# Performance work log

Measured on AMD Instinct MI355X. Metric: run time of the kernel, lower is better.

Reference implementation:

```python
import jax, jax.numpy as jnp
import numpy as np
import math

# Production-scale dims
B, C, H, W = 16, 3, 224, 224
STEPS = 32
T0, T1 = 0.0, 1.0
BETA = 0.1
IMPULSE = 1.0 / (abs(BETA) * math.sqrt(math.pi))
TSEQ = jnp.linspace(T0, T1, STEPS)  # sublevel thresholds


def _build_cells(x):
    """V-construction cubical complex over each [H,W] map.
    Cells: pixels (dim0, sign +1), horizontal/vertical edges (dim1, sign -1),
    unit squares (dim2, sign +1). Filtration value of a cell = max over its
    incident pixels (sublevel set / lower-star filtration).
    Returns (vals [B,C,N], pix [B,C,N] argmax pixel id, sign [N]).
    """
    b, c, h, w = x.shape
    hw = h * w
    pid = jnp.arange(hw, dtype=jnp.int32).reshape(h, w)
    # vertices (+1)
    v_vals = x.reshape(b, c, hw)
    v_pix = jnp.broadcast_to(pid.reshape(hw), (b, c, hw))
    # horizontal edges (-1)
    l, r = x[..., :, :-1], x[..., :, 1:]
    h_vals = jnp.maximum(l, r).reshape(b, c, -1)
    h_pix = jnp.where(l >= r, pid[:, :-1], pid[:, 1:]).reshape(b, c, -1)
    # vertical edges (-1)
    u, d = x[..., :-1, :], x[..., 1:, :]
    ve_vals = jnp.maximum(u, d).reshape(b, c, -1)
    ve_pix = jnp.where(u >= d, pid[:-1, :], pid[1:, :]).reshape(b, c, -1)
    # squares (+1): max over 2x2 block, track argmax corner pixel
    sq = jnp.stack([x[..., :-1, :-1], x[..., :-1, 1:], x[..., 1:, :-1], x[..., 1:, 1:]], axis=-1)
    sq_vals = sq.max(-1)
    am = sq.argmax(-1)
    pids = jnp.stack([pid[:-1, :-1], pid[:-1, 1:], pid[1:, :-1], pid[1:, 1:]], axis=-1)  # [h-1,w-1,4]
    sq_pix = jnp.take_along_axis(jnp.broadcast_to(pids, sq.shape), am[..., None], axis=-1)[..., 0]
    sq_vals = sq_vals.reshape(b, c, -1)
    sq_pix = sq_pix.reshape(b, c, -1)
    vals = jnp.concatenate([v_vals, h_vals, ve_vals, sq_vals], axis=-1)
    pix = jnp.concatenate([v_pix, h_pix, ve_pix, sq_pix], axis=-1).astype(jnp.int32)
    sign = jnp.concatenate([
        jnp.ones(v_vals.shape[-1], x.dtype),
        -jnp.ones(h_vals.shape[-1], x.dtype),
        -jnp.ones(ve_vals.shape[-1], x.dtype),
        jnp.ones(sq_vals.shape[-1], x.dtype),
    ])
    return vals, pix, sign


def _ecc_forward(x):
    """ECC(t_k) = sum over cells of sign * 1[filtration_value <= t_k],
    computed via value-bucketing + scatter-add + cumulative sum.
    Returns (ecc [B, C*STEPS], residuals for backward)."""
    b, c = x.shape[0], x.shape[1]
    vals, pix, sign = _build_cells(x)
    # first threshold index k with TSEQ[k] >= f; cells with f > T1 never appear
    bins = jnp.searchsorted(TSEQ, vals, side='left')  # [B,C,N]
    mask = bins < STEPS
    bins_c = jnp.minimum(bins, STEPS - 1)
    contrib = jnp.where(mask, sign, jnp.zeros((), x.dtype))  # [B,C,N]
    n = vals.shape[-1]
    rows = jnp.arange(b * c, dtype=jnp.int32)[:, None]
    hist = jnp.zeros((b * c, STEPS), x.dtype).at[rows, bins_c.reshape(b * c, n)].add(
        contrib.reshape(b * c, n))
    ecc = jnp.cumsum(hist, axis=-1)  # Euler characteristic curve
    return ecc.reshape(b, c * STEPS), (pix, bins, mask, sign)


def setup_inputs() -> dict:
    key = jax.random.key(0)
    x = jax.random.uniform(key, (B, C, H, W), dtype=jnp.float32)
    return {"x": x}


def reference(x):
    # sublevel=True -> no negation; postprocess = Identity; output flattened [B, C*STEPS]
    ecc, _ = _ecc_forward(x)
    return ecc
```

## Files before the change

### kernel.cpp

```cpp
#include <hip/hip_runtime.h>

#define H_ 224
#define W_ 224
#define NIMG 48
#define NBINS 33
#define JOBS_PER_IMG 112
#define NBLK (NIMG * JOBS_PER_IMG / 4)
#define BLKS_PER_IMG (JOBS_PER_IMG / 4)

__device__ __forceinline__ int bin_of(float x) {
    const float C = 1.0f / 31.0f;
    int k = (int)__builtin_ceilf(x * 31.0f);
    k = min(k, 32);
    if ((float)(k - 1) * C >= x) --k;
    else if ((float)k * C < x) ++k;
    return k;
}

__global__ __launch_bounds__(256) void ecc_hist(const float* __restrict__ x,
                                                int* __restrict__ gh) {
    __shared__ int hist[4][NBINS];
    const int tid = threadIdx.x;
    const int wave = tid >> 6;
    const int lane = tid & 63;

    if (lane < NBINS) hist[wave][lane] = 0;

    const int job  = blockIdx.x * 4 + wave;
    const int img  = job / JOBS_PER_IMG;
    const int jj   = job % JOBS_PER_IMG;
    const int rowg = jj >> 2;
    const int colg = jj & 3;
    const int col  = colg * 63 + lane;
    const bool produce = (lane < 63) && (col < W_);
    const bool hasR    = produce && (col < W_ - 1);
    const int  colc    = min(col, W_ - 1);

    const float* base = x + (size_t)img * (H_ * W_) + (size_t)(rowg * 8) * W_ + colc;
    int* hw = hist[wave];

    int bcur = bin_of(base[0]);
    const int r0 = rowg * 8;

#pragma unroll
    for (int ri = 0; ri < 8; ++ri) {
        const bool hasD = (r0 + ri < H_ - 1);
        int bnext = hasD ? bin_of(base[(ri + 1) * W_]) : 0;
        int sh = __shfl_down(bcur | (bnext << 16), 1, 64);
        int bR = sh & 0xffff, bDR = sh >> 16;
        if (hasD) {
            int e1 = max(bcur, bR);
            int e2 = max(bcur, bnext);
            if (hasR) {
                int lo = min(e1, e2), hi = max(e1, e2);
                int sq = max(hi, bDR);
                if (bcur != lo) { atomicAdd(&hw[bcur], 1); atomicAdd(&hw[lo], -1); }
                if (sq != hi)   { atomicAdd(&hw[sq], 1);   atomicAdd(&hw[hi], -1); }
            } else if (produce) {
                if (bcur != e2) { atomicAdd(&hw[bcur], 1); atomicAdd(&hw[e2], -1); }
            }
        } else {
            int e1 = max(bcur, bR);
            if (hasR) {
                if (bcur != e1) { atomicAdd(&hw[bcur], 1); atomicAdd(&hw[e1], -1); }
            } else if (produce) {
                atomicAdd(&hw[bcur], 1);
            }
        }
        bcur = bnext;
    }
    __syncthreads();

    if (tid < NBINS) {
        gh[blockIdx.x * NBINS + tid] =
            hist[0][tid] + hist[1][tid] + hist[2][tid] + hist[3][tid];
    }
}

__global__ __launch_bounds__(64) void ecc_final(const int* __restrict__ gh,
                                                float* __restrict__ out) {
    const int img = blockIdx.x;
    const int lane = threadIdx.x;
    if (lane < 32) {
        int v = 0;
        const int* base = gh + img * BLKS_PER_IMG * NBINS + lane;
#pragma unroll
        for (int s = 0; s < BLKS_PER_IMG; ++s) v += base[s * NBINS];
        for (int off = 1; off < 32; off <<= 1) {
            int n = __shfl_up(v, off, 64);
            if (lane >= off) v += n;
        }
        out[img * 32 + lane] = (float)v;
    }
}

extern "C" void kernel_launch(void* const* d_in, const int* in_sizes, int n_in,
                              void* d_out, int out_size, void* d_ws, size_t ws_size,
                              hipStream_t stream) {
    const float* x = (const float*)d_in[0];
    float* out = (float*)d_out;
    int* gh = (int*)d_ws;

    ecc_hist<<<NBLK, 256, 0, stream>>>(x, gh);
    ecc_final<<<NIMG, 64, 0, stream>>>(gh, out);
}
```

Baseline: 12.56 us.

## Fuse histogram and scan into one block-per-image kernel

Replaces the two-kernel scheme (many small histogram blocks writing partials to workspace, then a per-image reduce/scan kernel) with one 1024-thread block per image. Each of the 16 waves covers 56 rows of a column strip, and the block reduces the wave histograms in shared memory before doing the prefix scan. This removes the second launch and the global workspace round trip. In exchange, only 48 blocks run, so few compute units are used and each wave walks a much longer serial row loop.

```diff
diff --git a/kernel.cpp b/kernel.cpp
--- a/kernel.cpp
+++ b/kernel.cpp
@@ -4,9 +4,8 @@
 #define W_ 224
 #define NIMG 48
 #define NBINS 33
-#define JOBS_PER_IMG 112
-#define NBLK (NIMG * JOBS_PER_IMG / 4)
-#define BLKS_PER_IMG (JOBS_PER_IMG / 4)
+#define NW 16
+#define ROWS_PER 56
 
 __device__ __forceinline__ int bin_of(float x) {
     const float C = 1.0f / 31.0f;
@@ -17,33 +16,31 @@
     return k;
 }
 
-__global__ __launch_bounds__(256) void ecc_hist(const float* __restrict__ x,
-                                                int* __restrict__ gh) {
-    __shared__ int hist[4][NBINS];
+__global__ __launch_bounds__(1024) void ecc_fused(const float* __restrict__ x,
+                                                  float* __restrict__ out) {
+    __shared__ int hist[NW][NBINS];
     const int tid = threadIdx.x;
     const int wave = tid >> 6;
     const int lane = tid & 63;
 
     if (lane < NBINS) hist[wave][lane] = 0;
 
-    const int job  = blockIdx.x * 4 + wave;
-    const int img  = job / JOBS_PER_IMG;
-    const int jj   = job % JOBS_PER_IMG;
-    const int rowg = jj >> 2;
-    const int colg = jj & 3;
+    const int img  = blockIdx.x;
+    const int rowg = wave >> 2;
+    const int colg = wave & 3;
     const int col  = colg * 63 + lane;
     const bool produce = (lane < 63) && (col < W_);
     const bool hasR    = produce && (col < W_ - 1);
     const int  colc    = min(col, W_ - 1);
+    const int  r0      = rowg * ROWS_PER;
 
-    const float* base = x + (size_t)img * (H_ * W_) + (size_t)(rowg * 8) * W_ + colc;
+    const float* base = x + (size_t)img * (H_ * W_) + (size_t)r0 * W_ + colc;
     int* hw = hist[wave];
 
     int bcur = bin_of(base[0]);
-    const int r0 = rowg * 8;
 
-#pragma unroll
-    for (int ri = 0; ri < 8; ++ri) {
+#pragma unroll 8
+    for (int ri = 0; ri < ROWS_PER; ++ri) {
         const bool hasD = (r0 + ri < H_ - 1);
         int bnext = hasD ? bin_of(base[(ri + 1) * W_]) : 0;
         int sh = __shfl_down(bcur | (bnext << 16), 1, 64);
@@ -71,26 +68,15 @@
     }
     __syncthreads();
 
-    if (tid < NBINS) {
-        gh[blockIdx.x * NBINS + tid] =
-            hist[0][tid] + hist[1][tid] + hist[2][tid] + hist[3][tid];
-    }
-}
-
-__global__ __launch_bounds__(64) void ecc_final(const int* __restrict__ gh,
-                                                float* __restrict__ out) {
-    const int img = blockIdx.x;
-    const int lane = threadIdx.x;
-    if (lane < 32) {
+    if (tid < 32) {
         int v = 0;
-        const int* base = gh + img * BLKS_PER_IMG * NBINS + lane;
 #pragma unroll
-        for (int s = 0; s < BLKS_PER_IMG; ++s) v += base[s * NBINS];
+        for (int w = 0; w < NW; ++w) v += hist[w][tid];
         for (int off = 1; off < 32; off <<= 1) {
             int n = __shfl_up(v, off, 64);
-            if (lane >= off) v += n;
+            if (tid >= off) v += n;
         }
-        out[img * 32 + lane] = (float)v;
+        out[img * 32 + tid] = (float)v;
     }
 }
 
@@ -99,8 +85,5 @@
                               hipStream_t stream) {
     const float* x = (const float*)d_in[0];
     float* out = (float*)d_out;
-    int* gh = (int*)d_ws;
-
-    ecc_hist<<<NBLK, 256, 0, stream>>>(x, gh);
-    ecc_final<<<NIMG, 64, 0, stream>>>(gh, out);
+    ecc_fused<<<NIMG, 1024, 0, stream>>>(x, out);
 }
```

Result: slower. 25.71 us (+104.6%).

## Fuse histogram and final scan into one kernel with flag-based sync

Applied to the files above, without the earlier changes.

Merges the per-block histogram kernel and the per-image reduce/scan kernel into a single launch. Each block publishes its partial histogram and then sets a release flag. The first 48 blocks spin on the flags of their image's blocks before doing the reduction and prefix scan. This removes the second launch and the gap between kernels, but relies on co-residency of all blocks. The flags are also never reset between calls, so on repeat calls stale flags can let a reader proceed before the current partials are written.

```diff
diff --git a/kernel.cpp b/kernel.cpp
--- a/kernel.cpp
+++ b/kernel.cpp
@@ -5,8 +5,10 @@
 #define NIMG 48
 #define NBINS 33
 #define JOBS_PER_IMG 112
-#define NBLK (NIMG * JOBS_PER_IMG / 4)
-#define BLKS_PER_IMG (JOBS_PER_IMG / 4)
+#define WPB 4
+#define NBLK (NIMG * JOBS_PER_IMG / WPB)
+#define BLKS_PER_IMG (JOBS_PER_IMG / WPB)
+#define MAGIC 0x5ECCD0DE
 
 __device__ __forceinline__ int bin_of(float x) {
     const float C = 1.0f / 31.0f;
@@ -17,16 +19,19 @@
     return k;
 }
 
-__global__ __launch_bounds__(256) void ecc_hist(const float* __restrict__ x,
-                                                int* __restrict__ gh) {
-    __shared__ int hist[4][NBINS];
+__global__ __launch_bounds__(256) void ecc_onepass(const float* __restrict__ x,
+                                                   int* __restrict__ gh,
+                                                   int* __restrict__ flags,
+                                                   float* __restrict__ out) {
+    __shared__ int hist[WPB][NBINS];
     const int tid = threadIdx.x;
     const int wave = tid >> 6;
     const int lane = tid & 63;
 
     if (lane < NBINS) hist[wave][lane] = 0;
 
-    const int job  = blockIdx.x * 4 + wave;
+    const int blk  = blockIdx.x;
+    const int job  = blk * WPB + wave;
     const int img  = job / JOBS_PER_IMG;
     const int jj   = job % JOBS_PER_IMG;
     const int rowg = jj >> 2;
@@ -72,25 +77,36 @@
     __syncthreads();
 
     if (tid < NBINS) {
-        gh[blockIdx.x * NBINS + tid] =
+        gh[blk * NBINS + tid] =
             hist[0][tid] + hist[1][tid] + hist[2][tid] + hist[3][tid];
     }
-}
+    __syncthreads();
 
-__global__ __launch_bounds__(64) void ecc_final(const int* __restrict__ gh,
-                                                float* __restrict__ out) {
-    const int img = blockIdx.x;
-    const int lane = threadIdx.x;
-    if (lane < 32) {
-        int v = 0;
-        const int* base = gh + img * BLKS_PER_IMG * NBINS + lane;
+    if (tid == 0) {
+        __threadfence();
+        __hip_atomic_store(&flags[blk], MAGIC, __ATOMIC_RELEASE,
+                           __HIP_MEMORY_SCOPE_AGENT);
+    }
+
+    if (blk < NIMG) {
+        if (tid < BLKS_PER_IMG) {
+            while (__hip_atomic_load(&flags[blk * BLKS_PER_IMG + tid],
+                                     __ATOMIC_ACQUIRE,
+                                     __HIP_MEMORY_SCOPE_AGENT) != MAGIC) {
+            }
+        }
+        __syncthreads();
+        if (tid < 32) {
+            int v = 0;
+            const int* basep = gh + blk * BLKS_PER_IMG * NBINS + tid;
 #pragma unroll
-        for (int s = 0; s < BLKS_PER_IMG; ++s) v += base[s * NBINS];
-        for (int off = 1; off < 32; off <<= 1) {
-            int n = __shfl_up(v, off, 64);
-            if (lane >= off) v += n;
+            for (int s = 0; s < BLKS_PER_IMG; ++s) v += basep[s * NBINS];
+            for (int off = 1; off < 32; off <<= 1) {
+                int n = __shfl_up(v, off, 64);
+                if (tid >= off) v += n;
+            }
+            out[blk * 32 + tid] = (float)v;
         }
-        out[img * 32 + lane] = (float)v;
     }
 }
 
@@ -100,7 +116,7 @@
     const float* x = (const float*)d_in[0];
     float* out = (float*)d_out;
     int* gh = (int*)d_ws;
+    int* flags = gh + NBLK * NBINS;
 
-    ecc_hist<<<NBLK, 256, 0, stream>>>(x, gh);
-    ecc_final<<<NIMG, 64, 0, stream>>>(gh, out);
+    ecc_onepass<<<NBLK, 256, 0, stream>>>(x, gh, flags, out);
 }
```

Measured after the change: 42.76 us. +240.3%, slower.
